# Kernel tuning notes

Measured on AMD Instinct MI355X. Metric: run time of the kernel, lower is better.

Reference implementation:

```python
import jax, jax.numpy as jnp
import numpy as np

S, B, D = 2048, 2, 1024
H, DH = 16, 64
DFF = 4096
E, K = 4, 2
SCALE = 1.0 / (DH ** 0.5)


def _ln(x, g, b, eps):
    m = jnp.mean(x, axis=-1, keepdims=True)
    v = jnp.mean((x - m) ** 2, axis=-1, keepdims=True)
    return (x - m) * jax.lax.rsqrt(v + eps) * g + b


def setup_inputs() -> dict:
    key = jax.random.key(0)
    ks = jax.random.split(key, 12)
    s = lambda k, shape, fan: jax.random.normal(k, shape, jnp.float32) * (fan ** -0.5)
    return {
        "hidden_states": jax.random.normal(ks[0], (S, B, D), jnp.float32),
        "ln_in_g": jnp.ones((D,), jnp.float32), "ln_in_b": jnp.zeros((D,), jnp.float32),
        "Wq": s(ks[1], (D, H * DH), D),
        "Wkv": s(ks[2], (D, 2 * H * DH), D),
        "Wo": s(ks[3], (H * DH, D), H * DH),
        "ln_attn_g": jnp.ones((D,), jnp.float32), "ln_attn_b": jnp.zeros((D,), jnp.float32),
        "ln_post_g": jnp.ones((D,), jnp.float32), "ln_post_b": jnp.zeros((D,), jnp.float32),
        "Wg": s(ks[4], (D, E), D),
        "W1": s(ks[5], (E, D, DFF), D), "b1": jnp.zeros((E, DFF), jnp.float32),
        "W2": s(ks[6], (E, DFF, D), DFF), "b2": jnp.zeros((E, D), jnp.float32),
    }


def reference(hidden_states, ln_in_g, ln_in_b, Wq, Wkv, Wo, ln_attn_g, ln_attn_b,
              ln_post_g, ln_post_b, Wg, W1, b1, W2, b2):
    # --- input layernorm (eps=1e-6) ---
    h = _ln(hidden_states, ln_in_g, ln_in_b, 1e-6)  # [S,B,D]

    # --- MultiHeadAttn2 (post-lnorm, no mask, no mems) ---
    q = (h @ Wq).reshape(S, B, H, DH)
    k, v = jnp.split((h @ Wkv).reshape(S, B, H, 2 * DH), 2, axis=-1)
    score = jnp.einsum('ibnd,jbnd->ijbn', q, k) * SCALE      # [S,S,B,H]
    prob = jax.nn.softmax(score, axis=1)
    attn_vec = jnp.einsum('ijbn,jbnd->ibnd', prob, v).reshape(S, B, H * DH)
    attn_out = attn_vec @ Wo
    attention_output = _ln(h + attn_out, ln_attn_g, ln_attn_b, 1e-5)

    # --- residual + post-attention layernorm (eps=1e-6) ---
    layernorm_input = hidden_states + attention_output
    x = _ln(layernorm_input, ln_post_g, ln_post_b, 1e-6)

    # --- top-k MoE (E=4, k=2, no token dropping) ---
    xt = x.reshape(-1, D)                                     # [T,D]
    probs = jax.nn.softmax(xt @ Wg, axis=-1)                  # [T,E]
    topv, topi = jax.lax.top_k(probs, K)                      # [T,K]
    gates = topv / jnp.sum(topv, axis=-1, keepdims=True)
    cw = jnp.zeros_like(probs)
    for kk in range(K):  # small fixed K
        cw = cw + gates[:, kk:kk + 1] * jax.nn.one_hot(topi[:, kk], E, dtype=probs.dtype)
    hmid = jax.nn.gelu(jnp.einsum('td,edf->tef', xt, W1) + b1, approximate=False)
    y = jnp.einsum('tef,efd->ted', hmid, W2) + b2             # [T,E,D]
    moe_out = jnp.einsum('te,ted->td', cw, y).reshape(S, B, D)

    # load-balancing aux loss: E * sum(mean_probs * top1_fraction)
    me = jnp.mean(probs, axis=0)
    ce = jnp.mean(jax.nn.one_hot(topi[:, 0], E, dtype=probs.dtype), axis=0)
    moe_loss = E * jnp.sum(me * ce)

    output = layernorm_input + moe_out
    return output, moe_loss
```

## Files before the change

kernel.cpp:

```cpp
#include <hip/hip_runtime.h>
#include <cmath>

#define S_   2048
#define B_   2
#define D_   1024
#define H_   16
#define DH_  64
#define DFF_ 4096
#define E_   4
#define T_   4096
#define SCALE_ 0.125f

typedef __attribute__((ext_vector_type(8))) short short8;
typedef __attribute__((ext_vector_type(4))) float f32x4;
typedef __attribute__((ext_vector_type(4))) unsigned short u16x4;
typedef __attribute__((ext_vector_type(4))) unsigned int u32x4;

static __device__ __forceinline__ unsigned short f2bf(float f) {
  union { float f; unsigned int u; } v; v.f = f;
  unsigned int r = v.u + 0x7FFFu + ((v.u >> 16) & 1u);
  return (unsigned short)(r >> 16);
}

static __device__ __forceinline__ float bf2f(unsigned short u) {
  union { unsigned int u; float f; } v; v.u = (unsigned int)u << 16;
  return v.f;
}

static __device__ __forceinline__ f32x4 mfma16(short8 a, short8 b, f32x4 c) {
  return __builtin_amdgcn_mfma_f32_16x16x32_bf16(a, b, c, 0, 0, 0);
}

static __device__ __forceinline__ void gll16(const unsigned short* g, unsigned short* l) {
  __builtin_amdgcn_global_load_lds(
      (const __attribute__((address_space(1))) void*)g,
      (__attribute__((address_space(3))) void*)l, 16, 0, 0);
}

static __device__ __forceinline__ float gelu_f(float vv) {
  float u = 0.7978845608f * (vv + 0.044715f * vv * vv * vv);
  u = fminf(fmaxf(u, -9.0f), 9.0f);
  float e2 = __expf(2.0f * u);
  return vv * e2 * (1.0f / (e2 + 1.0f));
}

__global__ void transpose_cvt(const float* __restrict__ in, unsigned short* __restrict__ out,
                              int R, int C) {
  __shared__ float t[64][33];
  size_t boff = (size_t)blockIdx.z * R * C;
  in += boff; out += boff;
  int c0 = blockIdx.x * 32, r0 = blockIdx.y * 64;
  for (int i = threadIdx.y; i < 64; i += 8)
    t[i][threadIdx.x] = in[(size_t)(r0 + i) * C + c0 + threadIdx.x];
  __syncthreads();
  for (int i = threadIdx.y; i < 32; i += 8) {
    float v0 = t[2 * threadIdx.x][i], v1 = t[2 * threadIdx.x + 1][i];
    unsigned int pk = (unsigned int)f2bf(v0) | ((unsigned int)f2bf(v1) << 16);
    *(unsigned int*)(&out[(size_t)(c0 + i) * R + r0 + 2 * threadIdx.x]) = pk;
  }
}

__global__ void transpose_cvt_split(const float* __restrict__ in,
    unsigned short* __restrict__ outh, unsigned short* __restrict__ outl, int R, int C) {
  __shared__ float t[64][33];
  int c0 = blockIdx.x * 32, r0 = blockIdx.y * 64;
  for (int i = threadIdx.y; i < 64; i += 8)
    t[i][threadIdx.x] = in[(size_t)(r0 + i) * C + c0 + threadIdx.x];
  __syncthreads();
  for (int i = threadIdx.y; i < 32; i += 8) {
    float v0 = t[2 * threadIdx.x][i], v1 = t[2 * threadIdx.x + 1][i];
    unsigned short h0 = f2bf(v0), h1 = f2bf(v1);
    unsigned int hp = (unsigned int)h0 | ((unsigned int)h1 << 16);
    unsigned int lp = (unsigned int)f2bf(v0 - bf2f(h0)) |
                      ((unsigned int)f2bf(v1 - bf2f(h1)) << 16);
    size_t o = (size_t)(c0 + i) * R + r0 + 2 * threadIdx.x;
    *(unsigned int*)(&outh[o]) = hp;
    *(unsigned int*)(&outl[o]) = lp;
  }
}

__global__ __launch_bounds__(256) void v_transpose(
    const unsigned short* __restrict__ kvh, const unsigned short* __restrict__ kvl,
    unsigned short* __restrict__ vTh, unsigned short* __restrict__ vTl) {
  __shared__ unsigned short th[64][72], tl[64][72];
  int j0 = blockIdx.x * 64;
  int bh = blockIdx.y;
  int b = bh & 1, n = bh >> 1;
  int tid = threadIdx.x;
  int jr = tid >> 3, dc = (tid & 7) * 8;
  for (int it = 0; it < 2; ++it) {
    int jj = it * 32 + jr;
    size_t src = ((size_t)((j0 + jj) * 2 + b)) * 2048 + n * 128 + 64 + dc;
    *(short8*)(&th[jj][dc]) = *(const short8*)(kvh + src);
    *(short8*)(&tl[jj][dc]) = *(const short8*)(kvl + src);
  }
  __syncthreads();
  int dr = tid >> 3, jc = (tid & 7) * 8;
  for (int it = 0; it < 2; ++it) {
    int d = it * 32 + dr;
    short8 oh, ol;
    for (int u = 0; u < 8; ++u) { oh[u] = th[jc + u][d]; ol[u] = tl[jc + u][d]; }
    size_t dst = ((size_t)((b * 16 + n) * 64 + d)) * 2048 + j0 + jc;
    *(short8*)(vTh + dst) = oh;
    *(short8*)(vTl + dst) = ol;
  }
}

static __device__ __forceinline__ void block_reduce2(float& s, float& s2, float* sh) {
  __syncthreads();
  for (int off = 32; off; off >>= 1) { s += __shfl_down(s, off); s2 += __shfl_down(s2, off); }
  int w = threadIdx.x >> 6;
  if ((threadIdx.x & 63) == 0) { sh[w * 2] = s; sh[w * 2 + 1] = s2; }
  __syncthreads();
  s = sh[0] + sh[2] + sh[4] + sh[6];
  s2 = sh[1] + sh[3] + sh[5] + sh[7];
}

__global__ __launch_bounds__(256) void ln_in_kernel(const float* __restrict__ hid,
    const float* __restrict__ g, const float* __restrict__ b,
    float* __restrict__ h, unsigned short* __restrict__ hbh, unsigned short* __restrict__ hbl) {
  __shared__ float sh[8];
  int t = blockIdx.x, tid = threadIdx.x;
  size_t ro = (size_t)t * D_;
  f32x4 v = ((const f32x4*)(hid + ro))[tid];
  float s = v[0] + v[1] + v[2] + v[3];
  float s2 = v[0]*v[0] + v[1]*v[1] + v[2]*v[2] + v[3]*v[3];
  block_reduce2(s, s2, sh);
  float mean = s * (1.0f / D_);
  float var = s2 * (1.0f / D_) - mean * mean;
  float rstd = rsqrtf(var + 1e-6f);
  f32x4 gv = ((const f32x4*)g)[tid], bv = ((const f32x4*)b)[tid];
  f32x4 y; u16x4 yh, yl;
  for (int c = 0; c < 4; ++c) {
    float z = (v[c] - mean) * rstd * gv[c] + bv[c];
    y[c] = z; yh[c] = f2bf(z); yl[c] = f2bf(z - bf2f(yh[c]));
  }
  ((f32x4*)(h + ro))[tid] = y;
  ((u16x4*)(hbh + ro))[tid] = yh;
  ((u16x4*)(hbl + ro))[tid] = yl;
}

__global__ __launch_bounds__(256) void ln_fused_kernel(
    const float* __restrict__ hid, const float* __restrict__ h, const float* __restrict__ ao,
    const float* __restrict__ ga, const float* __restrict__ ba,
    const float* __restrict__ gp, const float* __restrict__ bp,
    float* __restrict__ out, float* __restrict__ x, unsigned short* __restrict__ xb) {
  __shared__ float sh[8];
  int t = blockIdx.x, tid = threadIdx.x;
  size_t ro = (size_t)t * D_;
  f32x4 hv = ((const f32x4*)(h + ro))[tid];
  f32x4 av = ((const f32x4*)(ao + ro))[tid];
  f32x4 a = hv + av;
  float s = a[0] + a[1] + a[2] + a[3];
  float s2 = a[0]*a[0] + a[1]*a[1] + a[2]*a[2] + a[3]*a[3];
  block_reduce2(s, s2, sh);
  float mean = s * (1.0f / D_);
  float var = s2 * (1.0f / D_) - mean * mean;
  float rstd = rsqrtf(var + 1e-5f);
  f32x4 lg = ((const f32x4*)ga)[tid], lb = ((const f32x4*)ba)[tid];
  f32x4 hidv = ((const f32x4*)(hid + ro))[tid];
  f32x4 li;
  for (int c = 0; c < 4; ++c) li[c] = hidv[c] + (a[c] - mean) * rstd * lg[c] + lb[c];
  ((f32x4*)(out + ro))[tid] = li;
  float s3 = li[0] + li[1] + li[2] + li[3];
  float s4 = li[0]*li[0] + li[1]*li[1] + li[2]*li[2] + li[3]*li[3];
  block_reduce2(s3, s4, sh);
  float mean2 = s3 * (1.0f / D_);
  float var2 = s4 * (1.0f / D_) - mean2 * mean2;
  float rstd2 = rsqrtf(var2 + 1e-6f);
  f32x4 g2 = ((const f32x4*)gp)[tid], b2v = ((const f32x4*)bp)[tid];
  f32x4 xv; u16x4 xbv;
  for (int c = 0; c < 4; ++c) { float z = (li[c] - mean2) * rstd2 * g2[c] + b2v[c]; xv[c] = z; xbv[c] = f2bf(z); }
  ((f32x4*)(x + ro))[tid] = xv;
  ((u16x4*)(xb + ro))[tid] = xbv;
}

__global__ __launch_bounds__(256) void qkv_gemm(
    const unsigned short* __restrict__ Ah, const unsigned short* __restrict__ Al,
    const unsigned short* __restrict__ WqTh, const unsigned short* __restrict__ WqTl,
    const unsigned short* __restrict__ WkvTh, const unsigned short* __restrict__ WkvTl,
    unsigned short* __restrict__ qh, unsigned short* __restrict__ ql,
    unsigned short* __restrict__ kvh, unsigned short* __restrict__ kvl) {
  const int K = 1024;
  int m0 = blockIdx.y * 128, n0g = blockIdx.x * 128;
  const unsigned short *Bh, *Bl;
  unsigned short *Ch, *Cl;
  int NC, n0;
  if (n0g < 1024) { Bh = WqTh; Bl = WqTl; Ch = qh; Cl = ql; NC = 1024; n0 = n0g; }
  else { Bh = WkvTh; Bl = WkvTl; Ch = kvh; Cl = kvl; NC = 2048; n0 = n0g - 1024; }
  __shared__ unsigned short pool2[16384];
  unsigned short* Ash = pool2;
  unsigned short* Asl = pool2 + 4096;
  unsigned short* Bsh = pool2 + 8192;
  unsigned short* Bsl = pool2 + 12288;
  int tid = threadIdx.x;
  int lane = tid & 63, w = tid >> 6;
  int quad = lane >> 4, l15 = lane & 15;
  int wm = (w >> 1) * 64, wn = (w & 1) * 64;
  f32x4 acc[4][4];
  for (int i = 0; i < 4; ++i) for (int j = 0; j < 4; ++j) acc[i][j] = 0;
  int rs0 = w * 32 + (lane >> 2), rs1 = rs0 + 16;
  int cofs = (lane & 3) * 8;
  const unsigned short* gah0 = Ah + (size_t)(m0 + rs0) * K + cofs;
  const unsigned short* gah1 = Ah + (size_t)(m0 + rs1) * K + cofs;
  const unsigned short* gal0 = Al + (size_t)(m0 + rs0) * K + cofs;
  const unsigned short* gal1 = Al + (size_t)(m0 + rs1) * K + cofs;
  const unsigned short* gbh0 = Bh + (size_t)(n0 + rs0) * K + cofs;
  const unsigned short* gbh1 = Bh + (size_t)(n0 + rs1) * K + cofs;
  const unsigned short* gbl0 = Bl + (size_t)(n0 + rs0) * K + cofs;
  const unsigned short* gbl1 = Bl + (size_t)(n0 + rs1) * K + cofs;
  unsigned short* lA0 = &Ash[(w * 2 + 0) * 512];
  unsigned short* lA1 = &Ash[(w * 2 + 1) * 512];
  unsigned short* lAl0 = &Asl[(w * 2 + 0) * 512];
  unsigned short* lAl1 = &Asl[(w * 2 + 1) * 512];
  unsigned short* lB0 = &Bsh[(w * 2 + 0) * 512];
  unsigned short* lB1 = &Bsh[(w * 2 + 1) * 512];
  unsigned short* lBl0 = &Bsl[(w * 2 + 0) * 512];
  unsigned short* lBl1 = &Bsl[(w * 2 + 1) * 512];
  for (int k0 = 0; k0 < K; k0 += 32) {
    __syncthreads();
    gll16(gah0 + k0, lA0); gll16(gah1 + k0, lA1);
    gll16(gal0 + k0, lAl0); gll16(gal1 + k0, lAl1);
    gll16(gbh0 + k0, lB0); gll16(gbh1 + k0, lB1);
    gll16(gbl0 + k0, lBl0); gll16(gbl1 + k0, lBl1);
    __syncthreads();
    short8 afh[4], afl[4], bfh[4], bfl[4];
    for (int i = 0; i < 4; ++i) {
      int o = (wm + i * 16 + l15) * 32 + quad * 8;
      afh[i] = *(const short8*)(&Ash[o]);
      afl[i] = *(const short8*)(&Asl[o]);
    }
    for (int j = 0; j < 4; ++j) {
      int o = (wn + j * 16 + l15) * 32 + quad * 8;
      bfh[j] = *(const short8*)(&Bsh[o]);
      bfl[j] = *(const short8*)(&Bsl[o]);
    }
    for (int i = 0; i < 4; ++i)
      for (int j = 0; j < 4; ++j) {
        f32x4 a = acc[i][j];
        a = mfma16(afh[i], bfl[j], a);
        a = mfma16(afl[i], bfh[j], a);
        a = mfma16(afh[i], bfh[j], a);
        acc[i][j] = a;
      }
  }
  __syncthreads();
  unsigned short* eph = &pool2[w * 1152];
  unsigned short* epl = &pool2[4608 + w * 1152];
  int row16 = lane >> 3, chunk = lane & 7;
  for (int i = 0; i < 4; ++i) {
    for (int j = 0; j < 4; ++j) {
      f32x4 a = acc[i][j];
      int lo = j * 16 + l15;
      for (int r = 0; r < 4; ++r) {
        unsigned short hb = f2bf(a[r]);
        eph[(quad * 4 + r) * 72 + lo] = hb;
        epl[(quad * 4 + r) * 72 + lo] = f2bf(a[r] - bf2f(hb));
      }
    }
    for (int it = 0; it < 2; ++it) {
      int rr = it * 8 + row16;
      size_t go = (size_t)(m0 + wm + i * 16 + rr) * NC + n0 + wn + chunk * 8;
      *(u32x4*)(&Ch[go]) = *(const u32x4*)(&eph[rr * 72 + chunk * 8]);
      *(u32x4*)(&Cl[go]) = *(const u32x4*)(&epl[rr * 72 + chunk * 8]);
    }
    __syncthreads();
  }
}

template<int MT>
__global__ __launch_bounds__(256) void gemm3f(
    const unsigned short* __restrict__ Ah, const unsigned short* __restrict__ Al,
    const unsigned short* __restrict__ Bh, const unsigned short* __restrict__ Bl,
    float* __restrict__ Cf, int N, int K) {
  int m0 = blockIdx.y * MT, n0 = blockIdx.x * 128;
  __shared__ unsigned short pool3[MT * 64 + 8192];
  unsigned short* Ash = pool3;
  unsigned short* Asl = pool3 + MT * 32;
  unsigned short* Bsh = pool3 + MT * 64;
  unsigned short* Bsl = pool3 + MT * 64 + 4096;
  int tid = threadIdx.x;
  int lane = tid & 63, w = tid >> 6;
  int quad = lane >> 4, l15 = lane & 15;
  int wm = (w >> 1) * (MT / 2), wn = (w & 1) * 64;
  constexpr int MI = MT / 32;
  f32x4 acc[MI][4];
  for (int i = 0; i < MI; ++i) for (int j = 0; j < 4; ++j) acc[i][j] = 0;
  constexpr int AI = MT / 64;
  int cofs = (lane & 3) * 8;
  const unsigned short* gah[AI]; const unsigned short* gal[AI];
  unsigned short *lAh[AI], *lAl[AI];
  for (int is = 0; is < AI; ++is) {
    int rs = w * (MT / 4) + is * 16 + (lane >> 2);
    gah[is] = Ah + (size_t)(m0 + rs) * K + cofs;
    gal[is] = Al + (size_t)(m0 + rs) * K + cofs;
    lAh[is] = &Ash[(w * AI + is) * 512];
    lAl[is] = &Asl[(w * AI + is) * 512];
  }
  int rsB0 = w * 32 + (lane >> 2), rsB1 = rsB0 + 16;
  const unsigned short* gbh0 = Bh + (size_t)(n0 + rsB0) * K + cofs;
  const unsigned short* gbh1 = Bh + (size_t)(n0 + rsB1) * K + cofs;
  const unsigned short* gbl0 = Bl + (size_t)(n0 + rsB0) * K + cofs;
  const unsigned short* gbl1 = Bl + (size_t)(n0 + rsB1) * K + cofs;
  unsigned short* lB0 = &Bsh[(w * 2 + 0) * 512];
  unsigned short* lB1 = &Bsh[(w * 2 + 1) * 512];
  unsigned short* lBl0 = &Bsl[(w * 2 + 0) * 512];
  unsigned short* lBl1 = &Bsl[(w * 2 + 1) * 512];
  for (int k0 = 0; k0 < K; k0 += 32) {
    __syncthreads();
    for (int is = 0; is < AI; ++is) { gll16(gah[is] + k0, lAh[is]); gll16(gal[is] + k0, lAl[is]); }
    gll16(gbh0 + k0, lB0); gll16(gbh1 + k0, lB1);
    gll16(gbl0 + k0, lBl0); gll16(gbl1 + k0, lBl1);
    __syncthreads();
    short8 afh[MI], afl[MI], bfh[4], bfl[4];
    for (int i = 0; i < MI; ++i) {
      int o = (wm + i * 16 + l15) * 32 + quad * 8;
      afh[i] = *(const short8*)(&Ash[o]);
      afl[i] = *(const short8*)(&Asl[o]);
    }
    for (int j = 0; j < 4; ++j) {
      int o = (wn + j * 16 + l15) * 32 + quad * 8;
      bfh[j] = *(const short8*)(&Bsh[o]);
      bfl[j] = *(const short8*)(&Bsl[o]);
    }
    for (int i = 0; i < MI; ++i)
      for (int j = 0; j < 4; ++j) {
        f32x4 a = acc[i][j];
        a = mfma16(afh[i], bfl[j], a);
        a = mfma16(afl[i], bfh[j], a);
        a = mfma16(afh[i], bfh[j], a);
        acc[i][j] = a;
      }
  }
  __syncthreads();
  float* epf = (float*)(pool3 + w * 2176);
  for (int i = 0; i < MI; ++i) {
    for (int j = 0; j < 4; ++j) {
      f32x4 a = acc[i][j];
      for (int r = 0; r < 4; ++r) epf[(quad * 4 + r) * 68 + j * 16 + l15] = a[r];
    }
    for (int it = 0; it < 4; ++it) {
      int rr = (lane >> 4) + it * 4;
      int ch = lane & 15;
      *(f32x4*)(&Cf[(size_t)(m0 + wm + i * 16 + rr) * N + n0 + wn + ch * 4]) =
          *(const f32x4*)(&epf[rr * 68 + ch * 4]);
    }
    __syncthreads();
  }
}

__global__ __launch_bounds__(256) void moe_up(
    const unsigned short* __restrict__ A, const unsigned short* __restrict__ W1T,
    unsigned short* __restrict__ hmid, int N, int K,
    const int* __restrict__ cnt, const int* __restrict__ offs,
    const int* __restrict__ list, const float* __restrict__ b1) {
  int e = blockIdx.y >> 5, mt = blockIdx.y & 31;
  int M = cnt[e];
  int m0 = mt * 128, n0 = blockIdx.x * 128;
  if (M == 0 || m0 >= M) return;
  const unsigned short* Bt = W1T + (size_t)e * DFF_ * D_;
  const int* liste = list + e * T_;
  const float* bias = b1 + (size_t)e * DFF_;
  size_t obase = (size_t)offs[e];
  __shared__ unsigned short pool[16384];
  unsigned short* As0 = pool;
  unsigned short* Bs0 = pool + 4096;
  unsigned short* As1 = pool + 8192;
  unsigned short* Bs1 = pool + 12288;
  int tid = threadIdx.x;
  int lane = tid & 63, w = tid >> 6;
  int quad = lane >> 4, l15 = lane & 15;
  int wm = (w >> 1) * 64, wn = (w & 1) * 64;
  f32x4 acc[4][4];
  for (int i = 0; i < 4; ++i) for (int j = 0; j < 4; ++j) acc[i][j] = 0;
  int rs0 = w * 32 + (lane >> 2), rs1 = rs0 + 16;
  int sw = ((lane & 3) ^ ((lane >> 3) & 3)) * 8;
  const unsigned short* ga0 = A + (size_t)liste[min(m0 + rs0, M - 1)] * K + sw;
  const unsigned short* ga1 = A + (size_t)liste[min(m0 + rs1, M - 1)] * K + sw;
  const unsigned short* gb0 = Bt + (size_t)(n0 + rs0) * K + sw;
  const unsigned short* gb1 = Bt + (size_t)(n0 + rs1) * K + sw;
  int so0 = (w * 2 + 0) * 512, so1 = (w * 2 + 1) * 512;
  int sq = (l15 >> 1) & 3;
  auto stage = [&](unsigned short* Ab, unsigned short* Bb, int k) {
    gll16(ga0 + k, Ab + so0); gll16(ga1 + k, Ab + so1);
    gll16(gb0 + k, Bb + so0); gll16(gb1 + k, Bb + so1);
  };
  auto compute = [&](const unsigned short* Ab, const unsigned short* Bb) {
    short8 af[4], bfr[4];
    for (int i = 0; i < 4; ++i)
      af[i] = *(const short8*)(&Ab[(wm + i * 16 + l15) * 32 + (quad ^ sq) * 8]);
    for (int j = 0; j < 4; ++j)
      bfr[j] = *(const short8*)(&Bb[(wn + j * 16 + l15) * 32 + (quad ^ sq) * 8]);
    for (int i = 0; i < 4; ++i)
      for (int j = 0; j < 4; ++j)
        acc[i][j] = mfma16(af[i], bfr[j], acc[i][j]);
  };
  stage(As0, Bs0, 0);
  __syncthreads();
  for (int k0 = 0; k0 < K; k0 += 64) {
    stage(As1, Bs1, k0 + 32);
    compute(As0, Bs0);
    __syncthreads();
    if (k0 + 64 < K) stage(As0, Bs0, k0 + 64);
    compute(As1, Bs1);
    __syncthreads();
  }
  unsigned short* ep = &pool[w * 1152];
  int row16 = lane >> 3, chunk = lane & 7;
  for (int i = 0; i < 4; ++i) {
    for (int j = 0; j < 4; ++j) {
      f32x4 a = acc[i][j];
      int colg = n0 + wn + j * 16 + l15;
      float bv = bias[colg];
      for (int r = 0; r < 4; ++r)
        ep[(quad * 4 + r) * 72 + j * 16 + l15] = f2bf(gelu_f(a[r] + bv));
    }
    for (int it = 0; it < 2; ++it) {
      int rr = it * 8 + row16;
      int rowg = m0 + wm + i * 16 + rr;
      if (rowg < M)
        *(u32x4*)(&hmid[(obase + rowg) * DFF_ + n0 + wn + chunk * 8]) =
            *(const u32x4*)(&ep[rr * 72 + chunk * 8]);
    }
  }
}

__global__ __launch_bounds__(256) void moe_down(
    const unsigned short* __restrict__ hmid, const unsigned short* __restrict__ W2T,
    int N, int K,
    const int* __restrict__ cnt, const int* __restrict__ offs,
    const int* __restrict__ list, const float* __restrict__ gatev,
    const float* __restrict__ b2, float* __restrict__ accum) {
  int e = blockIdx.y >> 5, mt = blockIdx.y & 31;
  int M = cnt[e];
  int m0 = mt * 128, n0 = blockIdx.x * 128;
  if (M == 0 || m0 >= M) return;
  const unsigned short* A = hmid + (size_t)offs[e] * DFF_;
  const unsigned short* Bt = W2T + (size_t)e * D_ * DFF_;
  const int* liste = list + e * T_;
  const float* gv = gatev + e * T_;
  const float* bias = b2 + (size_t)e * D_;
  __shared__ unsigned short pool[16384];
  unsigned short* As0 = pool;
  unsigned short* Bs0 = pool + 4096;
  unsigned short* As1 = pool + 8192;
  unsigned short* Bs1 = pool + 12288;
  int tid = threadIdx.x;
  int lane = tid & 63, w = tid >> 6;
  int quad = lane >> 4, l15 = lane & 15;
  int wm = (w >> 1) * 64, wn = (w & 1) * 64;
  f32x4 acc[4][4];
  for (int i = 0; i < 4; ++i) for (int j = 0; j < 4; ++j) acc[i][j] = 0;
  int rs0 = w * 32 + (lane >> 2), rs1 = rs0 + 16;
  int sw = ((lane & 3) ^ ((lane >> 3) & 3)) * 8;
  const unsigned short* ga0 = A + (size_t)min(m0 + rs0, M - 1) * K + sw;
  const unsigned short* ga1 = A + (size_t)min(m0 + rs1, M - 1) * K + sw;
  const unsigned short* gb0 = Bt + (size_t)(n0 + rs0) * K + sw;
  const unsigned short* gb1 = Bt + (size_t)(n0 + rs1) * K + sw;
  int so0 = (w * 2 + 0) * 512, so1 = (w * 2 + 1) * 512;
  int sq = (l15 >> 1) & 3;
  auto stage = [&](unsigned short* Ab, unsigned short* Bb, int k) {
    gll16(ga0 + k, Ab + so0); gll16(ga1 + k, Ab + so1);
    gll16(gb0 + k, Bb + so0); gll16(gb1 + k, Bb + so1);
  };
  auto compute = [&](const unsigned short* Ab, const unsigned short* Bb) {
    short8 af[4], bfr[4];
    for (int i = 0; i < 4; ++i)
      af[i] = *(const short8*)(&Ab[(wm + i * 16 + l15) * 32 + (quad ^ sq) * 8]);
    for (int j = 0; j < 4; ++j)
      bfr[j] = *(const short8*)(&Bb[(wn + j * 16 + l15) * 32 + (quad ^ sq) * 8]);
    for (int i = 0; i < 4; ++i)
      for (int j = 0; j < 4; ++j)
        acc[i][j] = mfma16(af[i], bfr[j], acc[i][j]);
  };
  stage(As0, Bs0, 0);
  __syncthreads();
  for (int k0 = 0; k0 < K; k0 += 64) {
    stage(As1, Bs1, k0 + 32);
    compute(As0, Bs0);
    __syncthreads();
    if (k0 + 64 < K) stage(As0, Bs0, k0 + 64);
    compute(As1, Bs1);
    __syncthreads();
  }
  for (int i = 0; i < 4; ++i) for (int j = 0; j < 4; ++j) {
    int row = m0 + wm + i * 16 + quad * 4;
    int col = n0 + wn + j * 16 + l15;
    f32x4 a = acc[i][j];
    float bv = bias[col];
    for (int r = 0; r < 4; ++r) if (row + r < M) {
      int tt = liste[row + r];
      float gg = gv[row + r];
      atomicAdd(&accum[(size_t)tt * D_ + col], gg * (a[r] + bv));
    }
  }
}

__global__ __launch_bounds__(256, 2) void attn_kernel(
    const unsigned short* __restrict__ qh, const unsigned short* __restrict__ ql,
    const unsigned short* __restrict__ kvh, const unsigned short* __restrict__ kvl,
    const unsigned short* __restrict__ vTh, const unsigned short* __restrict__ vTl,
    unsigned short* __restrict__ avh, unsigned short* __restrict__ avl) {
  int bh = blockIdx.x;
  int itile = blockIdx.y;
  int b = bh & 1, n = bh >> 1;
  __shared__ unsigned short Kh[2][4096], Kl[2][4096], Vh[2][4096], Vl[2][4096];
  __shared__ unsigned short Ps[4][1152];
  int tid = threadIdx.x;
  int w = tid >> 6, lane = tid & 63, quad = lane >> 4, l15 = lane & 15;
  int i_base = itile * 64 + w * 16;
  short8 qfh[2], qfl[2];
  {
    size_t qo = ((size_t)((i_base + l15) * B_ + b)) * 1024 + n * 64;
    qfh[0] = *(const short8*)(qh + qo + quad * 8);
    qfh[1] = *(const short8*)(qh + qo + 32 + quad * 8);
    qfl[0] = *(const short8*)(ql + qo + quad * 8);
    qfl[1] = *(const short8*)(ql + qo + 32 + quad * 8);
  }
  float m_i[4], l_i[4];
  f32x4 o[4];
  for (int r = 0; r < 4; ++r) { m_i[r] = -1e30f; l_i[r] = 0.0f; }
  for (int d = 0; d < 4; ++d) o[d] = 0;
  int jk = tid >> 3;
  int ck = (tid & 7) ^ (jk & 7);
  size_t kS = ((size_t)(jk * 2 + b)) * 2048 + (size_t)n * 128 + ck * 8;
  size_t vS = ((size_t)((b * 16 + n) * 64 + jk)) * 2048 + ck * 8;
  int ldst = tid * 8;
  unsigned short* psw = &Ps[w][0];
  gll16(kvh + kS, &Kh[0][ldst]);           gll16(kvh + kS + 131072, &Kh[0][2048 + ldst]);
  gll16(kvl + kS, &Kl[0][ldst]);           gll16(kvl + kS + 131072, &Kl[0][2048 + ldst]);
  gll16(vTh + vS, &Vh[0][ldst]);           gll16(vTh + vS + 65536, &Vh[0][2048 + ldst]);
  gll16(vTl + vS, &Vl[0][ldst]);           gll16(vTl + vS + 65536, &Vl[0][2048 + ldst]);
  __syncthreads();
  for (int jt = 0; jt < 32; ++jt) {
    int cur = jt & 1;
    if (jt < 31) {
      int nb = cur ^ 1;
      size_t ks2 = kS + (size_t)(jt + 1) * 262144;
      size_t vs2 = vS + (size_t)(jt + 1) * 64;
      gll16(kvh + ks2, &Kh[nb][ldst]);     gll16(kvh + ks2 + 131072, &Kh[nb][2048 + ldst]);
      gll16(kvl + ks2, &Kl[nb][ldst]);     gll16(kvl + ks2 + 131072, &Kl[nb][2048 + ldst]);
      gll16(vTh + vs2, &Vh[nb][ldst]);     gll16(vTh + vs2 + 65536, &Vh[nb][2048 + ldst]);
      gll16(vTl + vs2, &Vl[nb][ldst]);     gll16(vTl + vs2 + 65536, &Vl[nb][2048 + ldst]);
    }
    f32x4 sac[4];
    __builtin_amdgcn_s_setprio(1);
    for (int t4 = 0; t4 < 4; ++t4) {
      int j = t4 * 16 + l15;
      int base = j * 64;
      int c0 = (quad ^ (j & 7)) << 3;
      int c1 = ((quad | 4) ^ (j & 7)) << 3;
      short8 kh0 = *(const short8*)(&Kh[cur][base + c0]);
      short8 kh1 = *(const short8*)(&Kh[cur][base + c1]);
      short8 kl0 = *(const short8*)(&Kl[cur][base + c0]);
      short8 kl1 = *(const short8*)(&Kl[cur][base + c1]);
      f32x4 a = 0;
      a = mfma16(qfh[0], kl0, a);
      a = mfma16(qfh[1], kl1, a);
      a = mfma16(qfl[0], kh0, a);
      a = mfma16(qfl[1], kh1, a);
      a = mfma16(qfh[0], kh0, a);
      a = mfma16(qfh[1], kh1, a);
      sac[t4] = a;
    }
    __builtin_amdgcn_s_setprio(0);
    float p[4][4];
    float alpha[4];
    for (int r = 0; r < 4; ++r) {
      float m1 = fmaxf(fmaxf(sac[0][r], sac[1][r]), fmaxf(sac[2][r], sac[3][r])) * SCALE_;
      for (int off = 1; off < 16; off <<= 1) m1 = fmaxf(m1, __shfl_xor(m1, off, 16));
      float mnew = fmaxf(m_i[r], m1);
      alpha[r] = __expf(m_i[r] - mnew);
      m_i[r] = mnew;
      float rs = 0.f;
      for (int t4 = 0; t4 < 4; ++t4) {
        float pp = __expf(sac[t4][r] * SCALE_ - mnew);
        p[t4][r] = pp; rs += pp;
      }
      for (int off = 1; off < 16; off <<= 1) rs += __shfl_xor(rs, off, 16);
      l_i[r] = l_i[r] * alpha[r] + rs;
    }
    for (int d = 0; d < 4; ++d) for (int r = 0; r < 4; ++r) o[d][r] *= alpha[r];
    for (int t4 = 0; t4 < 4; ++t4) for (int r = 0; r < 4; ++r)
      psw[(quad * 4 + r) * 72 + t4 * 16 + l15] = f2bf(p[t4][r]);
    __builtin_amdgcn_s_setprio(1);
    for (int dblk = 0; dblk < 4; ++dblk) {
      f32x4 a = o[dblk];
      int d = dblk * 16 + l15;
      int vb = d * 64;
      for (int ks = 0; ks < 2; ++ks) {
        short8 pfh = *(const short8*)(&psw[l15 * 72 + ks * 32 + quad * 8]);
        int ch = ((ks * 4 + quad) ^ (d & 7)) << 3;
        short8 vfh = *(const short8*)(&Vh[cur][vb + ch]);
        short8 vfl = *(const short8*)(&Vl[cur][vb + ch]);
        a = mfma16(pfh, vfl, a);
        a = mfma16(pfh, vfh, a);
      }
      o[dblk] = a;
    }
    __builtin_amdgcn_s_setprio(0);
    __syncthreads();
  }
  {
    int row16 = lane >> 3, chunk = lane & 7;
    for (int d = 0; d < 4; ++d) for (int r = 0; r < 4; ++r) {
      float val = o[d][r] / l_i[r];
      psw[(quad * 4 + r) * 72 + d * 16 + l15] = f2bf(val);
    }
    for (int it = 0; it < 2; ++it) {
      int rr = it * 8 + row16;
      size_t go = ((size_t)((i_base + rr) * B_ + b)) * 1024 + n * 64 + chunk * 8;
      *(u32x4*)(&avh[go]) = *(const u32x4*)(&psw[rr * 72 + chunk * 8]);
    }
    __syncthreads();
    for (int d = 0; d < 4; ++d) for (int r = 0; r < 4; ++r) {
      float val = o[d][r] / l_i[r];
      unsigned short hb = f2bf(val);
      psw[(quad * 4 + r) * 72 + d * 16 + l15] = f2bf(val - bf2f(hb));
    }
    for (int it = 0; it < 2; ++it) {
      int rr = it * 8 + row16;
      size_t go = ((size_t)((i_base + rr) * B_ + b)) * 1024 + n * 64 + chunk * 8;
      *(u32x4*)(&avl[go]) = *(const u32x4*)(&psw[rr * 72 + chunk * 8]);
    }
  }
}

__global__ __launch_bounds__(256) void gate_kernel(const float* __restrict__ x,
    const float* __restrict__ Wg, int* __restrict__ cnt,
    float* __restrict__ me_sum, float* __restrict__ ce_sum,
    int* __restrict__ list, float* __restrict__ gatev) {
  __shared__ float sl[64][4];
  int w = threadIdx.x >> 6, lane = threadIdx.x & 63;
  int tbase = blockIdx.x * 64;
  for (int k = 0; k < 16; ++k) {
    int t = tbase + w * 16 + k;
    f32x4 acc = 0;
    const float* xr = x + (size_t)t * D_;
    for (int j = 0; j < 16; ++j) {
      int d = j * 64 + lane;
      float xd = xr[d];
      f32x4 wg = ((const f32x4*)Wg)[d];
      acc += xd * wg;
    }
    for (int c = 0; c < 4; ++c) {
      float vv = acc[c];
      for (int off = 32; off; off >>= 1) vv += __shfl_down(vv, off);
      if (lane == 0) sl[w * 16 + k][c] = vv;
    }
  }
  __syncthreads();
  if (w == 0) {
    int t = tbase + lane;
    float p[4];
    float mx = fmaxf(fmaxf(sl[lane][0], sl[lane][1]), fmaxf(sl[lane][2], sl[lane][3]));
    float sum = 0.f;
    for (int e = 0; e < 4; ++e) { p[e] = expf(sl[lane][e] - mx); sum += p[e]; }
    float inv = 1.0f / sum;
    for (int e = 0; e < 4; ++e) p[e] *= inv;
    int i0 = 0;
    for (int e = 1; e < 4; ++e) if (p[e] > p[i0]) i0 = e;
    int i1 = (i0 == 0) ? 1 : 0;
    for (int e = 0; e < 4; ++e) if (e != i0 && p[e] > p[i1]) i1 = e;
    float g0 = p[i0] / (p[i0] + p[i1]);
    float g1 = p[i1] / (p[i0] + p[i1]);
    for (int e = 0; e < 4; ++e) {
      float vv = p[e];
      for (int off = 32; off; off >>= 1) vv += __shfl_down(vv, off);
      if (lane == 0) atomicAdd(&me_sum[e], vv);
    }
    unsigned long long lbm = (1ull << lane) - 1;
    for (int e = 0; e < 4; ++e) {
      unsigned long long m0 = __ballot(i0 == e);
      int tot = __popcll(m0);
      int base = 0;
      if (lane == e && tot > 0) {
        base = atomicAdd(&cnt[e], tot);
        atomicAdd(&ce_sum[e], (float)tot);
      }
      base = __shfl(base, e);
      if (i0 == e) {
        int pos = base + __popcll(m0 & lbm);
        list[e * T_ + pos] = t;
        gatev[e * T_ + pos] = g0;
      }
      unsigned long long m1 = __ballot(i1 == e);
      int tot1 = __popcll(m1);
      int base1 = 0;
      if (lane == e && tot1 > 0) base1 = atomicAdd(&cnt[e], tot1);
      base1 = __shfl(base1, e);
      if (i1 == e) {
        int pos = base1 + __popcll(m1 & lbm);
        list[e * T_ + pos] = t;
        gatev[e * T_ + pos] = g1;
      }
    }
  }
}

__global__ void loss_offs_kernel(const float* __restrict__ me, const float* __restrict__ ce,
                                 const int* __restrict__ cnt, int* __restrict__ offs,
                                 float* __restrict__ out) {
  if (threadIdx.x == 0) {
    float l = 0.f;
    for (int e = 0; e < E_; ++e) l += (me[e] * (1.0f / T_)) * (ce[e] * (1.0f / T_));
    out[0] = (float)E_ * l;
    int o = 0;
    for (int e = 0; e < E_; ++e) { offs[e] = o; o += cnt[e]; }
  }
}

extern "C" void kernel_launch(void* const* d_in, const int* in_sizes, int n_in,
                              void* d_out, int out_size, void* d_ws, size_t ws_size,
                              hipStream_t stream) {
  const float* hid       = (const float*)d_in[0];
  const float* ln_in_g   = (const float*)d_in[1];
  const float* ln_in_b   = (const float*)d_in[2];
  const float* Wq        = (const float*)d_in[3];
  const float* Wkv       = (const float*)d_in[4];
  const float* Wo        = (const float*)d_in[5];
  const float* ln_attn_g = (const float*)d_in[6];
  const float* ln_attn_b = (const float*)d_in[7];
  const float* ln_post_g = (const float*)d_in[8];
  const float* ln_post_b = (const float*)d_in[9];
  const float* Wg        = (const float*)d_in[10];
  const float* W1        = (const float*)d_in[11];
  const float* b1        = (const float*)d_in[12];
  const float* W2        = (const float*)d_in[13];
  const float* b2        = (const float*)d_in[14];
  float* out = (float*)d_out;

  char* p = (char*)d_ws;
  size_t off = 0;
  auto alloc = [&](size_t bytes) -> void* {
    void* r = p + off; off += (bytes + 255) & ~(size_t)255; return r;
  };
  float* h        = (float*)alloc((size_t)T_ * D_ * 4);
  float* x        = (float*)alloc((size_t)T_ * D_ * 4);
  unsigned short* hmid_all = (unsigned short*)h;
  unsigned short* qh = (unsigned short*)alloc((size_t)T_ * 1024 * 2);
  unsigned short* ql = (unsigned short*)alloc((size_t)T_ * 1024 * 2);
  float* attn_out = (float*)qh;
  unsigned short* hbh = (unsigned short*)alloc((size_t)T_ * D_ * 2);
  unsigned short* hbl = (unsigned short*)alloc((size_t)T_ * D_ * 2);
  unsigned short* vTh = hbh;
  unsigned short* vTl = hbl;
  unsigned short* xb  = (unsigned short*)alloc((size_t)T_ * D_ * 2);
  unsigned short* kvh = (unsigned short*)alloc((size_t)T_ * 2048 * 2);
  unsigned short* kvl = (unsigned short*)alloc((size_t)T_ * 2048 * 2);
  unsigned short* W1T = kvh;
  unsigned short* avh = (unsigned short*)alloc((size_t)T_ * 1024 * 2);
  unsigned short* avl = (unsigned short*)alloc((size_t)T_ * 1024 * 2);
  unsigned short* W2T = avh;
  unsigned short* WqTh  = (unsigned short*)alloc((size_t)1024 * 1024 * 2);
  unsigned short* WqTl  = (unsigned short*)alloc((size_t)1024 * 1024 * 2);
  unsigned short* WkvTh = (unsigned short*)alloc((size_t)2048 * 1024 * 2);
  unsigned short* WkvTl = (unsigned short*)alloc((size_t)2048 * 1024 * 2);
  unsigned short* WoTh  = (unsigned short*)alloc((size_t)1024 * 1024 * 2);
  unsigned short* WoTl  = (unsigned short*)alloc((size_t)1024 * 1024 * 2);
  void* ghdr = alloc(256);
  int* cnt = (int*)ghdr;
  float* me_sum = (float*)ghdr + 4;
  float* ce_sum = (float*)ghdr + 8;
  int* offs = (int*)ghdr + 12;
  int* list = (int*)alloc((size_t)E_ * T_ * 4);
  float* gatev = (float*)alloc((size_t)E_ * T_ * 4);

  hipMemsetAsync(ghdr, 0, 64, stream);

  dim3 tb(32, 8);
  transpose_cvt_split<<<dim3(32, 16), tb, 0, stream>>>(Wq, WqTh, WqTl, 1024, 1024);
  transpose_cvt_split<<<dim3(64, 16), tb, 0, stream>>>(Wkv, WkvTh, WkvTl, 1024, 2048);
  transpose_cvt_split<<<dim3(32, 16), tb, 0, stream>>>(Wo, WoTh, WoTl, 1024, 1024);

  ln_in_kernel<<<T_, 256, 0, stream>>>(hid, ln_in_g, ln_in_b, h, hbh, hbl);

  qkv_gemm<<<dim3(24, 32), 256, 0, stream>>>(hbh, hbl, WqTh, WqTl, WkvTh, WkvTl,
      qh, ql, kvh, kvl);

  v_transpose<<<dim3(32, 32), 256, 0, stream>>>(kvh, kvl, vTh, vTl);

  attn_kernel<<<dim3(32, 32), 256, 0, stream>>>(qh, ql, kvh, kvl, vTh, vTl, avh, avl);

  gemm3f<64><<<dim3(8, 64), 256, 0, stream>>>(avh, avl, WoTh, WoTl, attn_out, 1024, 1024);

  ln_fused_kernel<<<T_, 256, 0, stream>>>(hid, h, attn_out, ln_attn_g, ln_attn_b,
      ln_post_g, ln_post_b, out, x, xb);

  gate_kernel<<<T_ / 64, 256, 0, stream>>>(x, Wg, cnt, me_sum, ce_sum, list, gatev);
  loss_offs_kernel<<<1, 64, 0, stream>>>(me_sum, ce_sum, cnt, offs, out + (size_t)T_ * D_);

  transpose_cvt<<<dim3(128, 16, 4), tb, 0, stream>>>(W1, W1T, 1024, 4096);
  transpose_cvt<<<dim3(32, 64, 4), tb, 0, stream>>>(W2, W2T, 4096, 1024);

  moe_up<<<dim3(32, 128), 256, 0, stream>>>(xb, W1T, hmid_all, DFF_, 1024,
      cnt, offs, list, b1);
  moe_down<<<dim3(8, 128), 256, 0, stream>>>(hmid_all, W2T, D_, DFF_,
      cnt, offs, list, gatev, b2, out);
}
```

Baseline: 880.0 us.

## Double-buffer QKV GEMM with swizzled LDS and add lazy-rescale flash softmax

```diff
diff --git a/kernel.cpp b/kernel.cpp
--- a/kernel.cpp
+++ b/kernel.cpp
@@ -186,13 +186,11 @@
   const unsigned short *Bh, *Bl;
   unsigned short *Ch, *Cl;
   int NC, n0;
-  if (n0g < 1024) { Bh = WqTh; Bl = WqTl; Ch = qh; Cl = ql; NC = 1024; n0 = n0g; }
-  else { Bh = WkvTh; Bl = WkvTl; Ch = kvh; Cl = kvl; NC = 2048; n0 = n0g - 1024; }
-  __shared__ unsigned short pool2[16384];
-  unsigned short* Ash = pool2;
-  unsigned short* Asl = pool2 + 4096;
-  unsigned short* Bsh = pool2 + 8192;
-  unsigned short* Bsl = pool2 + 12288;
+  float cscale;
+  if (n0g < 1024) { Bh = WqTh; Bl = WqTl; Ch = qh; Cl = ql; NC = 1024; n0 = n0g; cscale = SCALE_; }
+  else { Bh = WkvTh; Bl = WkvTl; Ch = kvh; Cl = kvl; NC = 2048; n0 = n0g - 1024; cscale = 1.0f; }
+  __shared__ unsigned short pool2[32768];
+  unsigned short* buf[2] = { pool2, pool2 + 16384 };
   int tid = threadIdx.x;
   int lane = tid & 63, w = tid >> 6;
   int quad = lane >> 4, l15 = lane & 15;
@@ -200,40 +198,34 @@
   f32x4 acc[4][4];
   for (int i = 0; i < 4; ++i) for (int j = 0; j < 4; ++j) acc[i][j] = 0;
   int rs0 = w * 32 + (lane >> 2), rs1 = rs0 + 16;
-  int cofs = (lane & 3) * 8;
-  const unsigned short* gah0 = Ah + (size_t)(m0 + rs0) * K + cofs;
-  const unsigned short* gah1 = Ah + (size_t)(m0 + rs1) * K + cofs;
-  const unsigned short* gal0 = Al + (size_t)(m0 + rs0) * K + cofs;
-  const unsigned short* gal1 = Al + (size_t)(m0 + rs1) * K + cofs;
-  const unsigned short* gbh0 = Bh + (size_t)(n0 + rs0) * K + cofs;
-  const unsigned short* gbh1 = Bh + (size_t)(n0 + rs1) * K + cofs;
-  const unsigned short* gbl0 = Bl + (size_t)(n0 + rs0) * K + cofs;
-  const unsigned short* gbl1 = Bl + (size_t)(n0 + rs1) * K + cofs;
-  unsigned short* lA0 = &Ash[(w * 2 + 0) * 512];
-  unsigned short* lA1 = &Ash[(w * 2 + 1) * 512];
-  unsigned short* lAl0 = &Asl[(w * 2 + 0) * 512];
-  unsigned short* lAl1 = &Asl[(w * 2 + 1) * 512];
-  unsigned short* lB0 = &Bsh[(w * 2 + 0) * 512];
-  unsigned short* lB1 = &Bsh[(w * 2 + 1) * 512];
-  unsigned short* lBl0 = &Bsl[(w * 2 + 0) * 512];
-  unsigned short* lBl1 = &Bsl[(w * 2 + 1) * 512];
-  for (int k0 = 0; k0 < K; k0 += 32) {
-    __syncthreads();
-    gll16(gah0 + k0, lA0); gll16(gah1 + k0, lA1);
-    gll16(gal0 + k0, lAl0); gll16(gal1 + k0, lAl1);
-    gll16(gbh0 + k0, lB0); gll16(gbh1 + k0, lB1);
-    gll16(gbl0 + k0, lBl0); gll16(gbl1 + k0, lBl1);
-    __syncthreads();
+  int sw = ((lane & 3) ^ ((lane >> 3) & 3)) * 8;
+  const unsigned short* gah0 = Ah + (size_t)(m0 + rs0) * K + sw;
+  const unsigned short* gah1 = Ah + (size_t)(m0 + rs1) * K + sw;
+  const unsigned short* gal0 = Al + (size_t)(m0 + rs0) * K + sw;
+  const unsigned short* gal1 = Al + (size_t)(m0 + rs1) * K + sw;
+  const unsigned short* gbh0 = Bh + (size_t)(n0 + rs0) * K + sw;
+  const unsigned short* gbh1 = Bh + (size_t)(n0 + rs1) * K + sw;
+  const unsigned short* gbl0 = Bl + (size_t)(n0 + rs0) * K + sw;
+  const unsigned short* gbl1 = Bl + (size_t)(n0 + rs1) * K + sw;
+  int so0 = (w * 2 + 0) * 512, so1 = (w * 2 + 1) * 512;
+  int sq = (l15 >> 1) & 3;
+  auto stage = [&](unsigned short* bb, int k) {
+    gll16(gah0 + k, bb + so0);         gll16(gah1 + k, bb + so1);
+    gll16(gal0 + k, bb + 4096 + so0);  gll16(gal1 + k, bb + 4096 + so1);
+    gll16(gbh0 + k, bb + 8192 + so0);  gll16(gbh1 + k, bb + 8192 + so1);
+    gll16(gbl0 + k, bb + 12288 + so0); gll16(gbl1 + k, bb + 12288 + so1);
+  };
+  auto compute = [&](const unsigned short* bb) {
     short8 afh[4], afl[4], bfh[4], bfl[4];
     for (int i = 0; i < 4; ++i) {
-      int o = (wm + i * 16 + l15) * 32 + quad * 8;
-      afh[i] = *(const short8*)(&Ash[o]);
-      afl[i] = *(const short8*)(&Asl[o]);
+      int o = (wm + i * 16 + l15) * 32 + ((quad ^ sq) * 8);
+      afh[i] = *(const short8*)(&bb[o]);
+      afl[i] = *(const short8*)(&bb[4096 + o]);
     }
     for (int j = 0; j < 4; ++j) {
-      int o = (wn + j * 16 + l15) * 32 + quad * 8;
-      bfh[j] = *(const short8*)(&Bsh[o]);
-      bfl[j] = *(const short8*)(&Bsl[o]);
+      int o = (wn + j * 16 + l15) * 32 + ((quad ^ sq) * 8);
+      bfh[j] = *(const short8*)(&bb[8192 + o]);
+      bfl[j] = *(const short8*)(&bb[12288 + o]);
     }
     for (int i = 0; i < 4; ++i)
       for (int j = 0; j < 4; ++j) {
@@ -243,8 +235,17 @@
         a = mfma16(afh[i], bfh[j], a);
         acc[i][j] = a;
       }
-  }
-  __syncthreads();
+  };
+  stage(buf[0], 0);
+  __syncthreads();
+  for (int k0 = 0; k0 < K; k0 += 64) {
+    stage(buf[1], k0 + 32);
+    compute(buf[0]);
+    __syncthreads();
+    if (k0 + 64 < K) stage(buf[0], k0 + 64);
+    compute(buf[1]);
+    __syncthreads();
+  }
   unsigned short* eph = &pool2[w * 1152];
   unsigned short* epl = &pool2[4608 + w * 1152];
   int row16 = lane >> 3, chunk = lane & 7;
@@ -253,9 +254,10 @@
       f32x4 a = acc[i][j];
       int lo = j * 16 + l15;
       for (int r = 0; r < 4; ++r) {
-        unsigned short hb = f2bf(a[r]);
+        float av = a[r] * cscale;
+        unsigned short hb = f2bf(av);
         eph[(quad * 4 + r) * 72 + lo] = hb;
-        epl[(quad * 4 + r) * 72 + lo] = f2bf(a[r] - bf2f(hb));
+        epl[(quad * 4 + r) * 72 + lo] = f2bf(av - bf2f(hb));
       }
     }
     for (int it = 0; it < 2; ++it) {
@@ -517,9 +519,9 @@
     qfl[0] = *(const short8*)(ql + qo + quad * 8);
     qfl[1] = *(const short8*)(ql + qo + 32 + quad * 8);
   }
-  float m_i[4], l_i[4];
+  float m_i[4], lp[4];
   f32x4 o[4];
-  for (int r = 0; r < 4; ++r) { m_i[r] = -1e30f; l_i[r] = 0.0f; }
+  for (int r = 0; r < 4; ++r) { m_i[r] = -1e30f; lp[r] = 0.0f; }
   for (int d = 0; d < 4; ++d) o[d] = 0;
   int jk = tid >> 3;
   int ck = (tid & 7) ^ (jk & 7);
@@ -564,23 +566,39 @@
       sac[t4] = a;
     }
     __builtin_amdgcn_s_setprio(0);
+    float m1[4];
+    for (int r = 0; r < 4; ++r) {
+      float v = fmaxf(fmaxf(sac[0][r], sac[1][r]), fmaxf(sac[2][r], sac[3][r]));
+      for (int off = 1; off < 16; off <<= 1) v = fmaxf(v, __shfl_xor(v, off, 16));
+      m1[r] = v;
+    }
     float p[4][4];
-    float alpha[4];
-    for (int r = 0; r < 4; ++r) {
-      float m1 = fmaxf(fmaxf(sac[0][r], sac[1][r]), fmaxf(sac[2][r], sac[3][r])) * SCALE_;
-      for (int off = 1; off < 16; off <<= 1) m1 = fmaxf(m1, __shfl_xor(m1, off, 16));
-      float mnew = fmaxf(m_i[r], m1);
-      alpha[r] = __expf(m_i[r] - mnew);
-      m_i[r] = mnew;
-      float rs = 0.f;
-      for (int t4 = 0; t4 < 4; ++t4) {
-        float pp = __expf(sac[t4][r] * SCALE_ - mnew);
-        p[t4][r] = pp; rs += pp;
+    bool ok = (m1[0] <= m_i[0] + 8.f) && (m1[1] <= m_i[1] + 8.f) &&
+              (m1[2] <= m_i[2] + 8.f) && (m1[3] <= m_i[3] + 8.f);
+    if (__all(ok)) {
+      for (int r = 0; r < 4; ++r) {
+        float rs = 0.f;
+        for (int t4 = 0; t4 < 4; ++t4) {
+          float pp = __expf(sac[t4][r] - m_i[r]);
+          p[t4][r] = pp; rs += pp;
+        }
+        lp[r] += rs;
       }
-      for (int off = 1; off < 16; off <<= 1) rs += __shfl_xor(rs, off, 16);
-      l_i[r] = l_i[r] * alpha[r] + rs;
-    }
-    for (int d = 0; d < 4; ++d) for (int r = 0; r < 4; ++r) o[d][r] *= alpha[r];
+    } else {
+      float alpha[4];
+      for (int r = 0; r < 4; ++r) {
+        float mnew = fmaxf(m_i[r], m1[r]);
+        alpha[r] = __expf(m_i[r] - mnew);
+        m_i[r] = mnew;
+        float rs = 0.f;
+        for (int t4 = 0; t4 < 4; ++t4) {
+          float pp = __expf(sac[t4][r] - mnew);
+          p[t4][r] = pp; rs += pp;
+        }
+        lp[r] = lp[r] * alpha[r] + rs;
+      }
+      for (int d = 0; d < 4; ++d) for (int r = 0; r < 4; ++r) o[d][r] *= alpha[r];
+    }
     for (int t4 = 0; t4 < 4; ++t4) for (int r = 0; r < 4; ++r)
       psw[(quad * 4 + r) * 72 + t4 * 16 + l15] = f2bf(p[t4][r]);
     __builtin_amdgcn_s_setprio(1);
@@ -600,6 +618,12 @@
     }
     __builtin_amdgcn_s_setprio(0);
     __syncthreads();
+  }
+  float l_i[4];
+  for (int r = 0; r < 4; ++r) {
+    float v = lp[r];
+    for (int off = 1; off < 16; off <<= 1) v += __shfl_xor(v, off, 16);
+    l_i[r] = v;
   }
   {
     int row16 = lane >> 3, chunk = lane & 7;
```

Result: faster. 826.0 us (-6.1%).
